# Kernel tuning notes

Measured on AMD Instinct MI355X. Metric: run time of the kernel, lower is better.

Reference implementation:

```python
import jax, jax.numpy as jnp
import numpy as np

N = 200000       # n_nodes
D = 128          # memory_dimension
E = 100000       # number of unique event source nodes this batch
OUTPUT = 30.0    # time-decay constant for embeddings
LAMB = 1.0 * OUTPUT  # self.lamb = lamb * output, used by memory updater
SLOPE = 0.01     # LeakyReLU default negative slope
EPS = 1e-10


def _leaky(x):
    return jnp.where(x >= 0, x, SLOPE * x)


def setup_inputs() -> dict:
    key = jax.random.key(0)
    ks = jax.random.split(key, 10)
    # memory: [N, D+1]; first D cols = exp-weighted message sum, last col = decayed event count (>=1)
    memory = jax.random.uniform(ks[0], (N, D + 1), dtype=jnp.float32)
    memory = memory.at[:, D].add(1.0)
    last_update = jax.random.uniform(ks[1], (N,), dtype=jnp.float32) * 50.0
    # unique sources (aggregator guarantees uniqueness) -> use a random permutation prefix
    unique_sources = jax.random.permutation(ks[2], N)[:E].astype(jnp.int32)
    unique_messages = jax.random.normal(ks[3], (E, D + 1), dtype=jnp.float32) * 0.1
    unique_messages = unique_messages.at[:, D].set(1.0)  # one event per message (ones column)
    # event times after last_update, before now_time
    unique_timestamps = jax.random.uniform(ks[4], (E,), dtype=jnp.float32) * 50.0 + 50.0
    now_time = jnp.float32(110.0)
    static_emb = jax.random.normal(ks[5], (N, D), dtype=jnp.float32) * 0.1
    W1 = jax.random.normal(ks[6], (2 * D, D), dtype=jnp.float32) / np.sqrt(2 * D)
    b1 = jnp.zeros((D,), dtype=jnp.float32)
    W2 = jax.random.normal(ks[7], (D, D), dtype=jnp.float32) / np.sqrt(D)
    b2 = jnp.zeros((D,), dtype=jnp.float32)
    e_lamb = jnp.float32(0.5)
    return {"memory": memory, "last_update": last_update, "unique_messages": unique_messages,
            "unique_timestamps": unique_timestamps, "static_emb": static_emb,
            "W1": W1, "b1": b1, "W2": W2, "b2": b2, "e_lamb": e_lamb,
            "now_time": now_time, "unique_sources": unique_sources}


def reference(memory, last_update, unique_messages, unique_timestamps, static_emb,
              W1, b1, W2, b2, e_lamb, now_time, unique_sources):
    # --- ExpMemoryUpdater.get_updated_memory: exp-decay old state, add new messages, bump last_update
    decay = jnp.exp((last_update[unique_sources] - unique_timestamps) / LAMB)  # [E]
    new_rows = memory[unique_sources] * decay[:, None] + unique_messages       # [E, D+1]
    upd_mem = memory.at[unique_sources].set(new_rows)                          # [N, D+1]
    upd_lu = last_update.at[unique_sources].set(unique_timestamps)             # [N]
    # --- ExpLambsEmbedding over all nodes: [sum/count, sum] -> cat -> [N, 2D]
    msum = upd_mem[:, :D]
    cnt = upd_mem[:, D:D + 1]
    feat = jnp.concatenate([msum / (cnt + EPS), msum], axis=-1)                # [N, 2D]
    # --- embedding_transform: Linear(2D->D) + LeakyReLU + Linear(D->D) + LeakyReLU
    h = _leaky(_leaky(feat @ W1 + b1) @ W2 + b2)                               # [N, D]
    # --- exponential time-decay to 'now'
    dec = h * jnp.exp((upd_lu - now_time) / OUTPUT)[:, None]                   # [N, D]
    # --- learned convex combination with static embedding table
    return e_lamb * static_emb + (1.0 - e_lamb) * dec
```

## Files before the change

kernel.cpp:

```cpp
#include <hip/hip_runtime.h>
#include <hip/hip_bf16.h>

#define N_ROWS 200000
#define DIMS   128
#define E_UPD  100000
#define TILE   64
#define NTILES (N_ROWS / TILE)
#define FSTRIDE 264
#define HSTRIDE 136
#define MAIN_GRID 768

typedef float f32x4 __attribute__((ext_vector_type(4)));
typedef __bf16 bf16x8 __attribute__((ext_vector_type(8)));
typedef unsigned short u16x8 __attribute__((ext_vector_type(8)));

static __device__ __forceinline__ unsigned short f2b(float f) {
    __hip_bfloat16 b = __float2bfloat16(f);
    return __builtin_bit_cast(unsigned short, b);
}

__global__ void fill_inv(int* inv, int* counter) {
    int i = blockIdx.x * blockDim.x + threadIdx.x;
    if (i < N_ROWS) inv[i] = -1;
    if (i == 0) counter[0] = 0;
}

__global__ void scatter_inv(const int* __restrict__ src, int* __restrict__ inv) {
    int e = blockIdx.x * blockDim.x + threadIdx.x;
    if (e < E_UPD) inv[src[e]] = e;
}

__launch_bounds__(512)
__global__ void ctdg_main(
    const float* __restrict__ memory,
    const float* __restrict__ last_update,
    const float* __restrict__ umsg,
    const float* __restrict__ uts,
    const float* __restrict__ semb,
    const float* __restrict__ W1,
    const float* __restrict__ b1,
    const float* __restrict__ W2,
    const float* __restrict__ b2,
    const float* __restrict__ e_lamb_p,
    const float* __restrict__ now_p,
    const int*   __restrict__ inv,
    int*         __restrict__ counter,
    float*       __restrict__ out)
{
    __shared__ __align__(16) unsigned short feat[TILE][FSTRIDE];
    __shared__ __align__(16) unsigned short h1s[TILE][HSTRIDE];
    __shared__ float rdecay[TILE];
    __shared__ float rcinv[TILE];
    __shared__ float rscale[TILE];
    __shared__ int   ridx[TILE];
    __shared__ int   s_tile;

    const int tid  = threadIdx.x;
    const int lane = tid & 63;
    const int wave = tid >> 6;
    const int quad = lane >> 4;
    const int l16  = lane & 15;
    const int wn   = wave * 16;

    u16x8 w1f[8];
    u16x8 w2f[4];
    #pragma unroll
    for (int t = 0; t < 8; ++t) {
        #pragma unroll
        for (int j = 0; j < 8; ++j)
            w1f[t][j] = f2b(W1[(t*32 + quad*8 + j)*128 + wn + l16]);
    }
    #pragma unroll
    for (int t = 0; t < 4; ++t) {
        #pragma unroll
        for (int j = 0; j < 8; ++j)
            w2f[t][j] = f2b(W2[(t*32 + quad*8 + j)*128 + wn + l16]);
    }
    const float b1v   = b1[wn + l16];
    const float b2v   = b2[wn + l16];
    const float el    = e_lamb_p[0];
    const float nowt  = now_p[0];
    const float inv30 = 1.0f / 30.0f;

    for (;;) {
        if (tid == 0) s_tile = atomicAdd(counter, 1);
        __syncthreads();
        const int tile = s_tile;
        if (tile >= NTILES) break;
        const int row0 = tile * TILE;

        if (tid < TILE) {
            const int g = row0 + tid;
            const float lu = last_update[g];
            const int e = inv[g];
            float dec = 1.0f, cnt, lun;
            const float mc = memory[(size_t)g*129 + 128];
            if (e >= 0) {
                const float ts = uts[e];
                dec = __expf((lu - ts) * inv30);
                cnt = fmaf(mc, dec, umsg[(size_t)e*129 + 128]);
                lun = ts;
            } else {
                cnt = mc;
                lun = lu;
            }
            rdecay[tid] = dec;
            rcinv[tid]  = 1.0f / (cnt + 1e-10f);
            rscale[tid] = __expf((lun - nowt) * inv30);
            ridx[tid]   = e;
        }
        __syncthreads();

        {
            const int r = tid >> 3;
            const int s = tid & 7;
            const int g = row0 + r;
            const float d  = rdecay[r];
            const float ci = rcinv[r];
            const int   e  = ridx[r];
            const float* mrow = memory + (size_t)g*129;
            if (e >= 0) {
                const float* grow = umsg + (size_t)e*129;
                #pragma unroll
                for (int j = 0; j < 16; ++j) {
                    const int c = s + j*8;
                    const float ms = fmaf(mrow[c], d, grow[c]);
                    feat[r][c]       = f2b(ms * ci);
                    feat[r][128 + c] = f2b(ms);
                }
            } else {
                #pragma unroll
                for (int j = 0; j < 16; ++j) {
                    const int c = s + j*8;
                    const float ms = mrow[c];
                    feat[r][c]       = f2b(ms * ci);
                    feat[r][128 + c] = f2b(ms);
                }
            }
        }
        __syncthreads();

        #pragma unroll
        for (int mt = 0; mt < 4; ++mt) {
            f32x4 acc = {0.f, 0.f, 0.f, 0.f};
            const int mrow = mt*16 + l16;
            #pragma unroll
            for (int k = 0; k < 8; ++k) {
                u16x8 a = *(const u16x8*)&feat[mrow][k*32 + quad*8];
                acc = __builtin_amdgcn_mfma_f32_16x16x32_bf16(
                        __builtin_bit_cast(bf16x8, a),
                        __builtin_bit_cast(bf16x8, w1f[k]), acc, 0, 0, 0);
            }
            #pragma unroll
            for (int r = 0; r < 4; ++r) {
                float v = acc[r] + b1v;
                v = (v >= 0.f) ? v : 0.01f * v;
                h1s[mt*16 + quad*4 + r][wn + l16] = f2b(v);
            }
        }
        __syncthreads();

        #pragma unroll
        for (int mt = 0; mt < 4; ++mt) {
            f32x4 acc = {0.f, 0.f, 0.f, 0.f};
            const int mrow = mt*16 + l16;
            #pragma unroll
            for (int k = 0; k < 4; ++k) {
                u16x8 a = *(const u16x8*)&h1s[mrow][k*32 + quad*8];
                acc = __builtin_amdgcn_mfma_f32_16x16x32_bf16(
                        __builtin_bit_cast(bf16x8, a),
                        __builtin_bit_cast(bf16x8, w2f[k]), acc, 0, 0, 0);
            }
            #pragma unroll
            for (int r = 0; r < 4; ++r) {
                const int row = mt*16 + quad*4 + r;
                const int g = row0 + row;
                float v = acc[r] + b2v;
                v = (v >= 0.f) ? v : 0.01f * v;
                v *= rscale[row];
                const float sv = semb[(size_t)g*128 + wn + l16];
                out[(size_t)g*128 + wn + l16] = el * sv + (1.0f - el) * v;
            }
        }
        __syncthreads();
    }
}

extern "C" void kernel_launch(void* const* d_in, const int* in_sizes, int n_in,
                              void* d_out, int out_size, void* d_ws, size_t ws_size,
                              hipStream_t stream) {
    const float* memory      = (const float*)d_in[0];
    const float* last_update = (const float*)d_in[1];
    const float* umsg        = (const float*)d_in[2];
    const float* uts         = (const float*)d_in[3];
    const float* semb        = (const float*)d_in[4];
    const float* W1          = (const float*)d_in[5];
    const float* b1          = (const float*)d_in[6];
    const float* W2          = (const float*)d_in[7];
    const float* b2          = (const float*)d_in[8];
    const float* e_lamb      = (const float*)d_in[9];
    const float* nowt        = (const float*)d_in[10];
    const int*   src         = (const int*)d_in[11];

    int* inv     = (int*)d_ws;
    int* counter = inv + N_ROWS;
    float* out   = (float*)d_out;

    fill_inv<<<(N_ROWS + 255) / 256, 256, 0, stream>>>(inv, counter);
    scatter_inv<<<(E_UPD + 255) / 256, 256, 0, stream>>>(src, inv);
    ctdg_main<<<MAIN_GRID, 512, 0, stream>>>(memory, last_update, umsg, uts, semb,
                                             W1, b1, W2, b2, e_lamb, nowt,
                                             inv, counter, out);
}
```

Baseline: 326.1 us.

## Halve row tile and flatten memory tile load for contiguous coalesced access

Row tiles shrink from 64 to 32 rows, the persistent grid grows from 768 to 1024 blocks, and the MFMA loops are trimmed to match. The feature-building stage now reads the tile's memory rows as one flat contiguous span indexed over all 512 threads, instead of each thread striding through a single row. This aims for fully coalesced loads of the odd 129-float rows and more blocks in flight to hide latency. The cost is a per-element divide by 129 and per-element lookups of the row's metadata, plus twice as many atomic tile grabs and barriers per row.

```diff
diff --git a/kernel.cpp b/kernel.cpp
--- a/kernel.cpp
+++ b/kernel.cpp
@@ -4,11 +4,11 @@
 #define N_ROWS 200000
 #define DIMS   128
 #define E_UPD  100000
-#define TILE   64
+#define TILE   32
 #define NTILES (N_ROWS / TILE)
 #define FSTRIDE 264
 #define HSTRIDE 136
-#define MAIN_GRID 768
+#define MAIN_GRID 1024
 
 typedef float f32x4 __attribute__((ext_vector_type(4)));
 typedef __bf16 bf16x8 __attribute__((ext_vector_type(8)));
@@ -112,36 +112,29 @@
         __syncthreads();
 
         {
-            const int r = tid >> 3;
-            const int s = tid & 7;
-            const int g = row0 + r;
-            const float d  = rdecay[r];
-            const float ci = rcinv[r];
-            const int   e  = ridx[r];
-            const float* mrow = memory + (size_t)g*129;
-            if (e >= 0) {
-                const float* grow = umsg + (size_t)e*129;
-                #pragma unroll
-                for (int j = 0; j < 16; ++j) {
-                    const int c = s + j*8;
-                    const float ms = fmaf(mrow[c], d, grow[c]);
-                    feat[r][c]       = f2b(ms * ci);
-                    feat[r][128 + c] = f2b(ms);
+            const float* tbase = memory + (size_t)row0 * 129;
+            #pragma unroll
+            for (int i = 0; i < 9; ++i) {
+                const int idx = i*512 + tid;
+                if (idx < TILE*129) {
+                    const float v = tbase[idx];
+                    const unsigned r = (unsigned)idx / 129u;
+                    const int c = idx - (int)r*129;
+                    if (c < 128) {
+                        const int e = ridx[r];
+                        float ms = v;
+                        if (e >= 0)
+                            ms = fmaf(v, rdecay[r], umsg[(size_t)e*129 + c]);
+                        feat[r][c]       = f2b(ms * rcinv[r]);
+                        feat[r][128 + c] = f2b(ms);
+                    }
                 }
-            } else {
-                #pragma unroll
-                for (int j = 0; j < 16; ++j) {
-                    const int c = s + j*8;
-                    const float ms = mrow[c];
-                    feat[r][c]       = f2b(ms * ci);
-                    feat[r][128 + c] = f2b(ms);
-                }
-            }
-        }
-        __syncthreads();
-
-        #pragma unroll
-        for (int mt = 0; mt < 4; ++mt) {
+            }
+        }
+        __syncthreads();
+
+        #pragma unroll
+        for (int mt = 0; mt < 2; ++mt) {
             f32x4 acc = {0.f, 0.f, 0.f, 0.f};
             const int mrow = mt*16 + l16;
             #pragma unroll
@@ -161,7 +154,7 @@
         __syncthreads();
 
         #pragma unroll
-        for (int mt = 0; mt < 4; ++mt) {
+        for (int mt = 0; mt < 2; ++mt) {
             f32x4 acc = {0.f, 0.f, 0.f, 0.f};
             const int mrow = mt*16 + l16;
             #pragma unroll
```

Measured after the change: 426.8 us. 30.9% more time.
